# Optimization experiments

Hardware: AMD Instinct MI355X
Metric: run time of the kernel (lower is better)

## Reference

```python
import jax, jax.numpy as jnp
import numpy as np

NUM_FEATURES = 16
EMBED_DIM = 8
D = NUM_FEATURES * EMBED_DIM  # 128
BATCH = 524288


def setup_inputs() -> dict:
    key = jax.random.key(0)
    ks = jax.random.split(key, 7)
    s = 1.0 / np.sqrt(D)
    return {
        "x": jax.random.normal(ks[0], (BATCH, D), dtype=jnp.float32),
        "Wk": jax.random.normal(ks[1], (D, D), dtype=jnp.float32) * s,
        "bk": jnp.zeros((D,), dtype=jnp.float32),
        "Wq": jax.random.normal(ks[2], (D, D), dtype=jnp.float32) * s,
        "bq": jnp.zeros((D,), dtype=jnp.float32),
        "Wv": jax.random.normal(ks[3], (D, D), dtype=jnp.float32) * s,
        "bv": jnp.zeros((D,), dtype=jnp.float32),
    }


def reference(x, Wk, bk, Wq, bq, Wv, bv):
    # Dense + exact gelu projections (keras 'gelu' activation is exact erf-gelu)
    gelu = lambda t: jax.nn.gelu(t, approximate=False)
    k = gelu(x @ Wk + bk)  # [B, D]
    q = gelu(x @ Wq + bq)
    v = gelu(x @ Wv + bv)
    B = x.shape[0]
    k = k.reshape(B, NUM_FEATURES, EMBED_DIM)
    q = q.reshape(B, NUM_FEATURES, EMBED_DIM)
    v = v.reshape(B, NUM_FEATURES, EMBED_DIM)
    # y = K^T Q : [B, E, E]; res = V y : [B, F, E]
    y = jnp.einsum('bfe,bfg->beg', k, q)
    res = jnp.einsum('bfe,beg->bfg', v, y)
    return res.reshape(B, D) + x
```

## Files before the change

### kernel.cpp

```cpp
#include <hip/hip_runtime.h>

typedef __bf16 bf16x8 __attribute__((ext_vector_type(8)));
typedef float f32x4 __attribute__((ext_vector_type(4)));
typedef float f32x2 __attribute__((ext_vector_type(2)));
typedef unsigned short ushort8 __attribute__((ext_vector_type(8)));
typedef unsigned int uint4v __attribute__((ext_vector_type(4)));
typedef unsigned int uint2v __attribute__((ext_vector_type(2)));

__device__ __forceinline__ unsigned short f2bf(float f){
    unsigned u = __float_as_uint(f);
    u += 0x7fffu + ((u >> 16) & 1u);
    return (unsigned short)(u >> 16);
}
__device__ __forceinline__ unsigned cvt_pk_bf16(float lo, float hi){
    unsigned r;
    asm("v_cvt_pk_bf16_f32 %0, %1, %2" : "=v"(r) : "v"(lo), "v"(hi));
    return r;
}
__device__ __forceinline__ float bflo(unsigned w){ return __uint_as_float(w << 16); }
__device__ __forceinline__ float bfhi(unsigned w){ return __uint_as_float(w & 0xffff0000u); }

__device__ __forceinline__ float gelu_tanh(float x){
    float x2 = x * x;
    float p  = fmaf(0.0356774081f, x2, 0.7978845608f);
    float t  = x * p;
    float e  = __expf(t + t);
    float r  = __builtin_amdgcn_rcpf(e + 1.0f);
    return fmaf(-x, r, x);
}

#define TM 64
#define LST 136

__global__ void pack_w_kernel(const float* __restrict__ Wk, const float* __restrict__ Wq,
                              const float* __restrict__ Wv, unsigned short* __restrict__ wp){
    int b = blockIdx.x;
    int lane = threadIdx.x;
    int p  = b >> 5;
    int ks = (b >> 3) & 3;
    int nf = b & 7;
    const float* W = (p == 0) ? Wk : ((p == 1) ? Wq : Wv);
    int k0  = ks * 32 + (lane >> 4) * 8;
    int col = nf * 16 + (lane & 15);
    unsigned short* dst = wp + ((size_t)b * 64 + lane) * 8;
    #pragma unroll
    for (int j = 0; j < 8; ++j) dst[j] = f2bf(W[(size_t)(k0 + j) * 128 + col]);
}

__global__ __launch_bounds__(256, 3) void fused_tcross(
        const float* __restrict__ x, const unsigned short* __restrict__ wp,
        const float* __restrict__ bk, const float* __restrict__ bq,
        const float* __restrict__ bv, float* __restrict__ out){
    __shared__ __align__(16) unsigned short smem[3 * TM * LST];

    const int tid  = threadIdx.x;
    const int lane = tid & 63;
    const int wave = tid >> 6;
    const int c16  = lane & 15;
    const int kg   = lane >> 4;
    const long long row0 = (long long)blockIdx.x * TM;

    float bpre0[2], bpre1[2], bpre2[2];
    #pragma unroll
    for (int j = 0; j < 2; ++j){
        int col = (wave * 2 + j) * 16 + c16;
        bpre0[j] = bv[col];
        bpre1[j] = bq[col];
        bpre2[j] = bk[col];
    }

    const float* xblk = x + row0 * 128;
    f32x4 resid[8];
    #pragma unroll
    for (int it = 0; it < 8; ++it){
        int e = tid * 4 + it * 1024;
        f32x4 v = *(const f32x4*)(xblk + e);
        resid[it] = v;
        uint2v w;
        w[0] = cvt_pk_bf16(v[0], v[1]);
        w[1] = cvt_pk_bf16(v[2], v[3]);
        *(uint2v*)&smem[(e >> 7) * LST + (e & 127)] = w;
    }
    __syncthreads();

    const int pack_p[3] = {2, 1, 0};
    const int plane[3]  = {2, 1, 0};
    #pragma unroll
    for (int pi = 0; pi < 3; ++pi){
        f32x4 acc[4][2];
        const f32x4 zero = {0.f, 0.f, 0.f, 0.f};
        #pragma unroll
        for (int m = 0; m < 4; ++m){ acc[m][0] = zero; acc[m][1] = zero; }
        #pragma unroll
        for (int ks = 0; ks < 4; ++ks){
            bf16x8 af[4];
            #pragma unroll
            for (int m = 0; m < 4; ++m)
                af[m] = __builtin_bit_cast(bf16x8,
                    *(const ushort8*)&smem[(m * 16 + c16) * LST + ks * 32 + kg * 8]);
            #pragma unroll
            for (int j = 0; j < 2; ++j){
                const int nf = wave * 2 + j;
                const size_t fidx = ((size_t)((pack_p[pi] * 4 + ks) * 8 + nf) * 64 + lane) * 8;
                bf16x8 wfrag = __builtin_bit_cast(bf16x8, *(const ushort8*)(wp + fidx));
                #pragma unroll
                for (int m = 0; m < 4; ++m)
                    acc[m][j] = __builtin_amdgcn_mfma_f32_16x16x32_bf16(
                        af[m], wfrag, acc[m][j], 0, 0, 0);
            }
        }
        if (pi == 2) __syncthreads();
        unsigned short* sp = smem + plane[pi] * TM * LST;
        const float bb0 = (pi == 0) ? bpre0[0] : ((pi == 1) ? bpre1[0] : bpre2[0]);
        const float bb1 = (pi == 0) ? bpre0[1] : ((pi == 1) ? bpre1[1] : bpre2[1]);
        #pragma unroll
        for (int j = 0; j < 2; ++j){
            const int col = (wave * 2 + j) * 16 + c16;
            const float bb = j ? bb1 : bb0;
            #pragma unroll
            for (int m = 0; m < 4; ++m){
                float g0 = gelu_tanh(acc[m][j][0] + bb);
                float g1 = gelu_tanh(acc[m][j][1] + bb);
                float g2 = gelu_tanh(acc[m][j][2] + bb);
                float g3 = gelu_tanh(acc[m][j][3] + bb);
                unsigned u01 = cvt_pk_bf16(g0, g1);
                unsigned u23 = cvt_pk_bf16(g2, g3);
                const int r = m * 16 + kg * 4;
                sp[(r + 0) * LST + col] = (unsigned short)u01;
                sp[(r + 1) * LST + col] = (unsigned short)(u01 >> 16);
                sp[(r + 2) * LST + col] = (unsigned short)u23;
                sp[(r + 3) * LST + col] = (unsigned short)(u23 >> 16);
            }
        }
    }
    __syncthreads();

    const int row = tid >> 2;
    const int sub = tid & 3;
    const unsigned short* krow = smem + 0 * TM * LST + row * LST;
    const unsigned short* qrow = smem + 1 * TM * LST + row * LST;
    const unsigned short* vrow = smem + 2 * TM * LST + row * LST;

    f32x2 y2[8];
    #pragma unroll
    for (int e = 0; e < 8; ++e) y2[e] = (f32x2){0.f, 0.f};
    #pragma unroll
    for (int f = 0; f < 16; ++f){
        uint4v ku = *(const uint4v*)(krow + f * 8);
        unsigned qw = *(const unsigned*)(qrow + f * 8 + sub * 2);
        f32x2 qq = {bflo(qw), bfhi(qw)};
        float kf[8] = {bflo(ku[0]), bfhi(ku[0]), bflo(ku[1]), bfhi(ku[1]),
                       bflo(ku[2]), bfhi(ku[2]), bflo(ku[3]), bfhi(ku[3])};
        #pragma unroll
        for (int e = 0; e < 8; ++e){
            f32x2 kk = {kf[e], kf[e]};
            y2[e] += kk * qq;
        }
    }
    f32x2 rr[16];
    #pragma unroll
    for (int f = 0; f < 16; ++f){
        uint4v vu = *(const uint4v*)(vrow + f * 8);
        float vf[8] = {bflo(vu[0]), bfhi(vu[0]), bflo(vu[1]), bfhi(vu[1]),
                       bflo(vu[2]), bfhi(vu[2]), bflo(vu[3]), bfhi(vu[3])};
        f32x2 a = {0.f, 0.f};
        #pragma unroll
        for (int e = 0; e < 8; ++e){
            f32x2 vv = {vf[e], vf[e]};
            a += vv * y2[e];
        }
        rr[f] = a;
    }
    __syncthreads();

    float* s_res = (float*)smem;
    #pragma unroll
    for (int f = 0; f < 16; ++f)
        *(f32x2*)&s_res[row * LST + f * 8 + sub * 2] = rr[f];
    __syncthreads();

    float* outb = out + row0 * 128;
    #pragma unroll
    for (int it = 0; it < 8; ++it){
        int e = tid * 4 + it * 1024;
        f32x4 rv = *(const f32x4*)&s_res[(e >> 7) * LST + (e & 127)];
        rv += resid[it];
        *(f32x4*)(outb + e) = rv;
    }
}

extern "C" void kernel_launch(void* const* d_in, const int* in_sizes, int n_in,
                              void* d_out, int out_size, void* d_ws, size_t ws_size,
                              hipStream_t stream){
    const float* x  = (const float*)d_in[0];
    const float* Wk = (const float*)d_in[1];
    const float* bk = (const float*)d_in[2];
    const float* Wq = (const float*)d_in[3];
    const float* bq = (const float*)d_in[4];
    const float* Wv = (const float*)d_in[5];
    const float* bv = (const float*)d_in[6];
    float* out = (float*)d_out;
    unsigned short* wp = (unsigned short*)d_ws;

    const int B = in_sizes[0] / 128;

    pack_w_kernel<<<96, 64, 0, stream>>>(Wk, Wq, Wv, wp);
    fused_tcross<<<B / TM, 256, 0, stream>>>(x, wp, bk, bq, bv, out);

    (void)n_in; (void)out_size; (void)ws_size;
}
```

Measured before the change: 170.8 us.

## Use fp16 dot2 for the cross-feature stage and double threads per block

Stores the GELU outputs as fp16 rather than bf16, with K and Q written transposed in LDS. The two small einsums then run on v_dot2_f32_f16 packed dot products instead of unpacked fp32 FMAs. The block grows from 256 to 512 threads (8 waves), so each wave takes a 2x2 MFMA tile and each thread handles one output column group per row. The intermediate y is rounded to fp16, which adds precision risk, and the projection loop is no longer unrolled.

```diff
diff --git a/kernel.cpp b/kernel.cpp
--- a/kernel.cpp
+++ b/kernel.cpp
@@ -2,7 +2,7 @@
 
 typedef __bf16 bf16x8 __attribute__((ext_vector_type(8)));
 typedef float f32x4 __attribute__((ext_vector_type(4)));
-typedef float f32x2 __attribute__((ext_vector_type(2)));
+typedef __fp16 fp16x2 __attribute__((ext_vector_type(2)));
 typedef unsigned short ushort8 __attribute__((ext_vector_type(8)));
 typedef unsigned int uint4v __attribute__((ext_vector_type(4)));
 typedef unsigned int uint2v __attribute__((ext_vector_type(2)));
@@ -17,8 +17,19 @@
     asm("v_cvt_pk_bf16_f32 %0, %1, %2" : "=v"(r) : "v"(lo), "v"(hi));
     return r;
 }
-__device__ __forceinline__ float bflo(unsigned w){ return __uint_as_float(w << 16); }
-__device__ __forceinline__ float bfhi(unsigned w){ return __uint_as_float(w & 0xffff0000u); }
+__device__ __forceinline__ unsigned cvt_pk_f16(float lo, float hi){
+    return __builtin_bit_cast(unsigned, __builtin_amdgcn_cvt_pkrtz(lo, hi));
+}
+__device__ __forceinline__ float fdot2(unsigned a, unsigned b, float c){
+#if __has_builtin(__builtin_amdgcn_fdot2)
+    return __builtin_amdgcn_fdot2(__builtin_bit_cast(fp16x2, a),
+                                  __builtin_bit_cast(fp16x2, b), c, false);
+#else
+    float d;
+    asm("v_dot2_f32_f16 %0, %1, %2, %3" : "=v"(d) : "v"(a), "v"(b), "v"(c));
+    return d;
+#endif
+}
 
 __device__ __forceinline__ float gelu_tanh(float x){
     float x2 = x * x;
@@ -47,7 +58,7 @@
     for (int j = 0; j < 8; ++j) dst[j] = f2bf(W[(size_t)(k0 + j) * 128 + col]);
 }
 
-__global__ __launch_bounds__(256, 3) void fused_tcross(
+__global__ __launch_bounds__(512, 4) void fused_tcross(
         const float* __restrict__ x, const unsigned short* __restrict__ wp,
         const float* __restrict__ bk, const float* __restrict__ bq,
         const float* __restrict__ bv, float* __restrict__ out){
@@ -58,22 +69,24 @@
     const int wave = tid >> 6;
     const int c16  = lane & 15;
     const int kg   = lane >> 4;
+    const int wm   = wave & 1;
+    const int wn   = wave >> 1;
     const long long row0 = (long long)blockIdx.x * TM;
 
-    float bpre0[2], bpre1[2], bpre2[2];
-    #pragma unroll
-    for (int j = 0; j < 2; ++j){
-        int col = (wave * 2 + j) * 16 + c16;
-        bpre0[j] = bv[col];
-        bpre1[j] = bq[col];
-        bpre2[j] = bk[col];
+    float bpv[2], bpq[2], bpk[2];
+    #pragma unroll
+    for (int jj = 0; jj < 2; ++jj){
+        int col = (2 * wn + jj) * 16 + c16;
+        bpv[jj] = bv[col];
+        bpq[jj] = bq[col];
+        bpk[jj] = bk[col];
     }
 
     const float* xblk = x + row0 * 128;
-    f32x4 resid[8];
-    #pragma unroll
-    for (int it = 0; it < 8; ++it){
-        int e = tid * 4 + it * 1024;
+    f32x4 resid[4];
+    #pragma unroll
+    for (int it = 0; it < 4; ++it){
+        int e = tid * 4 + it * 2048;
         f32x4 v = *(const f32x4*)(xblk + e);
         resid[it] = v;
         uint2v w;
@@ -83,92 +96,86 @@
     }
     __syncthreads();
 
-    const int pack_p[3] = {2, 1, 0};
-    const int plane[3]  = {2, 1, 0};
-    #pragma unroll
+    #pragma unroll 1
     for (int pi = 0; pi < 3; ++pi){
-        f32x4 acc[4][2];
+        const int pp = 2 - pi;
+        f32x4 acc[2][2];
         const f32x4 zero = {0.f, 0.f, 0.f, 0.f};
-        #pragma unroll
-        for (int m = 0; m < 4; ++m){ acc[m][0] = zero; acc[m][1] = zero; }
+        acc[0][0] = zero; acc[0][1] = zero; acc[1][0] = zero; acc[1][1] = zero;
         #pragma unroll
         for (int ks = 0; ks < 4; ++ks){
-            bf16x8 af[4];
+            bf16x8 af[2];
             #pragma unroll
-            for (int m = 0; m < 4; ++m)
-                af[m] = __builtin_bit_cast(bf16x8,
-                    *(const ushort8*)&smem[(m * 16 + c16) * LST + ks * 32 + kg * 8]);
+            for (int mm = 0; mm < 2; ++mm)
+                af[mm] = __builtin_bit_cast(bf16x8, *(const ushort8*)
+                    &smem[((2 * wm + mm) * 16 + c16) * LST + ks * 32 + kg * 8]);
             #pragma unroll
-            for (int j = 0; j < 2; ++j){
-                const int nf = wave * 2 + j;
-                const size_t fidx = ((size_t)((pack_p[pi] * 4 + ks) * 8 + nf) * 64 + lane) * 8;
-                bf16x8 wfrag = __builtin_bit_cast(bf16x8, *(const ushort8*)(wp + fidx));
+            for (int jj = 0; jj < 2; ++jj){
+                const int nf = 2 * wn + jj;
+                const size_t fidx = ((size_t)((pp * 4 + ks) * 8 + nf) * 64 + lane) * 8;
+                bf16x8 wf = __builtin_bit_cast(bf16x8, *(const ushort8*)(wp + fidx));
                 #pragma unroll
-                for (int m = 0; m < 4; ++m)
-                    acc[m][j] = __builtin_amdgcn_mfma_f32_16x16x32_bf16(
-                        af[m], wfrag, acc[m][j], 0, 0, 0);
+                for (int mm = 0; mm < 2; ++mm)
+                    acc[mm][jj] = __builtin_amdgcn_mfma_f32_16x16x32_bf16(
+                        af[mm], wf, acc[mm][jj], 0, 0, 0);
             }
         }
         if (pi == 2) __syncthreads();
-        unsigned short* sp = smem + plane[pi] * TM * LST;
-        const float bb0 = (pi == 0) ? bpre0[0] : ((pi == 1) ? bpre1[0] : bpre2[0]);
-        const float bb1 = (pi == 0) ? bpre0[1] : ((pi == 1) ? bpre1[1] : bpre2[1]);
-        #pragma unroll
-        for (int j = 0; j < 2; ++j){
-            const int col = (wave * 2 + j) * 16 + c16;
-            const float bb = j ? bb1 : bb0;
+        unsigned short* sp = smem + (2 - pi) * TM * LST;
+        #pragma unroll
+        for (int jj = 0; jj < 2; ++jj){
+            const int col = (2 * wn + jj) * 16 + c16;
+            const int dcol = (pi == 0) ? col : ((col & 7) * 16 + (col >> 3));
+            const float bb = (pi == 0) ? bpv[jj] : ((pi == 1) ? bpq[jj] : bpk[jj]);
             #pragma unroll
-            for (int m = 0; m < 4; ++m){
-                float g0 = gelu_tanh(acc[m][j][0] + bb);
-                float g1 = gelu_tanh(acc[m][j][1] + bb);
-                float g2 = gelu_tanh(acc[m][j][2] + bb);
-                float g3 = gelu_tanh(acc[m][j][3] + bb);
-                unsigned u01 = cvt_pk_bf16(g0, g1);
-                unsigned u23 = cvt_pk_bf16(g2, g3);
-                const int r = m * 16 + kg * 4;
-                sp[(r + 0) * LST + col] = (unsigned short)u01;
-                sp[(r + 1) * LST + col] = (unsigned short)(u01 >> 16);
-                sp[(r + 2) * LST + col] = (unsigned short)u23;
-                sp[(r + 3) * LST + col] = (unsigned short)(u23 >> 16);
+            for (int mm = 0; mm < 2; ++mm){
+                float g0 = gelu_tanh(acc[mm][jj][0] + bb);
+                float g1 = gelu_tanh(acc[mm][jj][1] + bb);
+                float g2 = gelu_tanh(acc[mm][jj][2] + bb);
+                float g3 = gelu_tanh(acc[mm][jj][3] + bb);
+                unsigned u01 = cvt_pk_f16(g0, g1);
+                unsigned u23 = cvt_pk_f16(g2, g3);
+                const int r = (2 * wm + mm) * 16 + kg * 4;
+                sp[(r + 0) * LST + dcol] = (unsigned short)u01;
+                sp[(r + 1) * LST + dcol] = (unsigned short)(u01 >> 16);
+                sp[(r + 2) * LST + dcol] = (unsigned short)u23;
+                sp[(r + 3) * LST + dcol] = (unsigned short)(u23 >> 16);
             }
         }
     }
     __syncthreads();
 
-    const int row = tid >> 2;
-    const int sub = tid & 3;
-    const unsigned short* krow = smem + 0 * TM * LST + row * LST;
-    const unsigned short* qrow = smem + 1 * TM * LST + row * LST;
-    const unsigned short* vrow = smem + 2 * TM * LST + row * LST;
-
-    f32x2 y2[8];
-    #pragma unroll
-    for (int e = 0; e < 8; ++e) y2[e] = (f32x2){0.f, 0.f};
+    const int row = tid >> 3;
+    const int g   = tid & 7;
+    const unsigned short* kT = smem + 0 * TM * LST + row * LST;
+    const unsigned short* qT = smem + 1 * TM * LST + row * LST;
+    const unsigned short* vI = smem + 2 * TM * LST + row * LST;
+
+    uint4v qa = *(const uint4v*)(qT + g * 16);
+    uint4v qb = *(const uint4v*)(qT + g * 16 + 8);
+    float y[8];
+    #pragma unroll
+    for (int e = 0; e < 8; ++e){
+        uint4v ka = *(const uint4v*)(kT + e * 16);
+        uint4v kb = *(const uint4v*)(kT + e * 16 + 8);
+        float a = 0.f;
+        #pragma unroll
+        for (int j = 0; j < 4; ++j) a = fdot2(ka[j], qa[j], a);
+        #pragma unroll
+        for (int j = 0; j < 4; ++j) a = fdot2(kb[j], qb[j], a);
+        y[e] = a;
+    }
+    unsigned yp[4];
+    #pragma unroll
+    for (int i = 0; i < 4; ++i)
+        yp[i] = cvt_pk_f16(y[2*i], y[2*i+1]);
+    float rr[16];
     #pragma unroll
     for (int f = 0; f < 16; ++f){
-        uint4v ku = *(const uint4v*)(krow + f * 8);
-        unsigned qw = *(const unsigned*)(qrow + f * 8 + sub * 2);
-        f32x2 qq = {bflo(qw), bfhi(qw)};
-        float kf[8] = {bflo(ku[0]), bfhi(ku[0]), bflo(ku[1]), bfhi(ku[1]),
-                       bflo(ku[2]), bfhi(ku[2]), bflo(ku[3]), bfhi(ku[3])};
-        #pragma unroll
-        for (int e = 0; e < 8; ++e){
-            f32x2 kk = {kf[e], kf[e]};
-            y2[e] += kk * qq;
-        }
-    }
-    f32x2 rr[16];
-    #pragma unroll
-    for (int f = 0; f < 16; ++f){
-        uint4v vu = *(const uint4v*)(vrow + f * 8);
-        float vf[8] = {bflo(vu[0]), bfhi(vu[0]), bflo(vu[1]), bfhi(vu[1]),
-                       bflo(vu[2]), bfhi(vu[2]), bflo(vu[3]), bfhi(vu[3])};
-        f32x2 a = {0.f, 0.f};
-        #pragma unroll
-        for (int e = 0; e < 8; ++e){
-            f32x2 vv = {vf[e], vf[e]};
-            a += vv * y2[e];
-        }
+        uint4v vv = *(const uint4v*)(vI + f * 8);
+        float a = 0.f;
+        #pragma unroll
+        for (int i = 0; i < 4; ++i) a = fdot2(vv[i], yp[i], a);
         rr[f] = a;
     }
     __syncthreads();
@@ -176,13 +183,13 @@
     float* s_res = (float*)smem;
     #pragma unroll
     for (int f = 0; f < 16; ++f)
-        *(f32x2*)&s_res[row * LST + f * 8 + sub * 2] = rr[f];
+        s_res[row * LST + f * 8 + g] = rr[f];
     __syncthreads();
 
     float* outb = out + row0 * 128;
     #pragma unroll
-    for (int it = 0; it < 8; ++it){
-        int e = tid * 4 + it * 1024;
+    for (int it = 0; it < 4; ++it){
+        int e = tid * 4 + it * 2048;
         f32x4 rv = *(const f32x4*)&s_res[(e >> 7) * LST + (e & 127)];
         rv += resid[it];
         *(f32x4*)(outb + e) = rv;
@@ -205,7 +212,7 @@
     const int B = in_sizes[0] / 128;
 
     pack_w_kernel<<<96, 64, 0, stream>>>(Wk, Wq, Wv, wp);
-    fused_tcross<<<B / TM, 256, 0, stream>>>(x, wp, bk, bq, bv, out);
+    fused_tcross<<<B / TM, 512, 0, stream>>>(x, wp, bk, bq, bv, out);
 
     (void)n_in; (void)out_size; (void)ws_size;
 }
```

Result: slower. 182.2 us (+6.7%).

## Use polynomial GELU and fp16 dot2 for the V·Y contraction

Applied to the files above, without the earlier changes.

Replaces the tanh-based GELU, which needs an exp and a reciprocal, with a clamped polynomial in x² that uses only FMAs. The V projection is now stored as fp16 instead of bf16, and Y is packed to fp16, so V·Y can use v_dot2_f32_f16 rather than unpacking to fp32 and doing scalar FMAs. The projection loop is no longer unrolled (unroll 1), which should reduce code size and register pressure. The cost is precision: the polynomial approximates GELU, and fp16 packing of Y may overflow or lose accuracy when values are large.

```diff
diff --git a/kernel.cpp b/kernel.cpp
--- a/kernel.cpp
+++ b/kernel.cpp
@@ -3,6 +3,7 @@
 typedef __bf16 bf16x8 __attribute__((ext_vector_type(8)));
 typedef float f32x4 __attribute__((ext_vector_type(4)));
 typedef float f32x2 __attribute__((ext_vector_type(2)));
+typedef __fp16 fp16x2 __attribute__((ext_vector_type(2)));
 typedef unsigned short ushort8 __attribute__((ext_vector_type(8)));
 typedef unsigned int uint4v __attribute__((ext_vector_type(4)));
 typedef unsigned int uint2v __attribute__((ext_vector_type(2)));
@@ -17,16 +18,29 @@
     asm("v_cvt_pk_bf16_f32 %0, %1, %2" : "=v"(r) : "v"(lo), "v"(hi));
     return r;
 }
+__device__ __forceinline__ unsigned cvt_pk_f16(float lo, float hi){
+    return __builtin_bit_cast(unsigned, __builtin_amdgcn_cvt_pkrtz(lo, hi));
+}
+__device__ __forceinline__ float fdot2(unsigned a, unsigned b, float c){
+#if __has_builtin(__builtin_amdgcn_fdot2)
+    return __builtin_amdgcn_fdot2(__builtin_bit_cast(fp16x2, a),
+                                  __builtin_bit_cast(fp16x2, b), c, false);
+#else
+    float d;
+    asm("v_dot2_f32_f16 %0, %1, %2, %3" : "=v"(d) : "v"(a), "v"(b), "v"(c));
+    return d;
+#endif
+}
 __device__ __forceinline__ float bflo(unsigned w){ return __uint_as_float(w << 16); }
 __device__ __forceinline__ float bfhi(unsigned w){ return __uint_as_float(w & 0xffff0000u); }
 
-__device__ __forceinline__ float gelu_tanh(float x){
-    float x2 = x * x;
-    float p  = fmaf(0.0356774081f, x2, 0.7978845608f);
-    float t  = x * p;
-    float e  = __expf(t + t);
-    float r  = __builtin_amdgcn_rcpf(e + 1.0f);
-    return fmaf(-x, r, x);
+__device__ __forceinline__ float gelu_poly(float x){
+    float t = x * x;
+    float h = fmaf(fmaf(fmaf(fmaf(2.66044e-5f, t, -7.46798e-4f), t,
+                             9.014181e-3f), t, -6.5889388e-2f), t, 0.39894228f);
+    float p = fmaf(x, h, 0.5f);
+    p = fminf(fmaxf(p, 0.0f), 1.0f);
+    return x * p;
 }
 
 #define TM 64
@@ -85,7 +99,7 @@
 
     const int pack_p[3] = {2, 1, 0};
     const int plane[3]  = {2, 1, 0};
-    #pragma unroll
+    #pragma unroll 1
     for (int pi = 0; pi < 3; ++pi){
         f32x4 acc[4][2];
         const f32x4 zero = {0.f, 0.f, 0.f, 0.f};
@@ -119,12 +133,12 @@
             const float bb = j ? bb1 : bb0;
             #pragma unroll
             for (int m = 0; m < 4; ++m){
-                float g0 = gelu_tanh(acc[m][j][0] + bb);
-                float g1 = gelu_tanh(acc[m][j][1] + bb);
-                float g2 = gelu_tanh(acc[m][j][2] + bb);
-                float g3 = gelu_tanh(acc[m][j][3] + bb);
-                unsigned u01 = cvt_pk_bf16(g0, g1);
-                unsigned u23 = cvt_pk_bf16(g2, g3);
+                float g0 = gelu_poly(acc[m][j][0] + bb);
+                float g1 = gelu_poly(acc[m][j][1] + bb);
+                float g2 = gelu_poly(acc[m][j][2] + bb);
+                float g3 = gelu_poly(acc[m][j][3] + bb);
+                unsigned u01 = (pi == 0) ? cvt_pk_f16(g0, g1) : cvt_pk_bf16(g0, g1);
+                unsigned u23 = (pi == 0) ? cvt_pk_f16(g2, g3) : cvt_pk_bf16(g2, g3);
                 const int r = m * 16 + kg * 4;
                 sp[(r + 0) * LST + col] = (unsigned short)u01;
                 sp[(r + 1) * LST + col] = (unsigned short)(u01 >> 16);
@@ -157,19 +171,23 @@
             y2[e] += kk * qq;
         }
     }
+    unsigned yp0[4], yp1[4];
+    #pragma unroll
+    for (int i = 0; i < 4; ++i){
+        yp0[i] = cvt_pk_f16(y2[2*i][0], y2[2*i+1][0]);
+        yp1[i] = cvt_pk_f16(y2[2*i][1], y2[2*i+1][1]);
+    }
     f32x2 rr[16];
     #pragma unroll
     for (int f = 0; f < 16; ++f){
-        uint4v vu = *(const uint4v*)(vrow + f * 8);
-        float vf[8] = {bflo(vu[0]), bfhi(vu[0]), bflo(vu[1]), bfhi(vu[1]),
-                       bflo(vu[2]), bfhi(vu[2]), bflo(vu[3]), bfhi(vu[3])};
-        f32x2 a = {0.f, 0.f};
-        #pragma unroll
-        for (int e = 0; e < 8; ++e){
-            f32x2 vv = {vf[e], vf[e]};
-            a += vv * y2[e];
-        }
-        rr[f] = a;
+        uint4v vv = *(const uint4v*)(vrow + f * 8);
+        float a0 = 0.f, a1 = 0.f;
+        #pragma unroll
+        for (int i = 0; i < 4; ++i){
+            a0 = fdot2(vv[i], yp0[i], a0);
+            a1 = fdot2(vv[i], yp1[i], a1);
+        }
+        rr[f] = (f32x2){a0, a1};
     }
     __syncthreads();
 
```

Result: no change. 168.9 us (-1.1%).
